# Kernel tuning notes

Hardware: AMD Instinct MI355X
Metric: run time of the kernel (lower is better)

## Reference

```python
import jax, jax.numpy as jnp
import numpy as np

H = 1024  # hidden_size == embedding_size


def setup_inputs() -> dict:
    key = jax.random.key(0)
    ks = jax.random.split(key, 14)
    B, T, L, V = 2, 1, 8192, 50000
    emb_table = jax.random.normal(ks[0], (V, H), jnp.float32)
    emb_table = emb_table.at[0].set(0.0)  # row 0 zeroed as in the torch module
    return {
        "input_ids": jax.random.randint(ks[1], (B, T), 0, V),
        "last_context": jax.random.normal(ks[2], (B, T, H), jnp.float32),
        "last_hidden": jax.random.normal(ks[3], (1, B, H), jnp.float32),
        "encoder_outputs": jax.random.normal(ks[4], (B, L, H), jnp.float32),
        "emb_table": emb_table,
        "w_ih": jax.random.normal(ks[5], (3 * H, 2 * H), jnp.float32) * 0.02,
        "w_hh": jax.random.normal(ks[6], (3 * H, H), jnp.float32) * 0.02,
        "b_ih": jax.random.normal(ks[7], (3 * H,), jnp.float32) * 0.02,
        "b_hh": jax.random.normal(ks[8], (3 * H,), jnp.float32) * 0.02,
        "attn_w": jax.random.normal(ks[9], (H, 2 * H), jnp.float32) * 0.02,
        "attn_b": jax.random.normal(ks[10], (H,), jnp.float32) * 0.02,
        "v": jax.random.normal(ks[11], (H,), jnp.float32),
        "out_w": jax.random.normal(ks[12], (50000, 2 * H), jnp.float32) * 0.02,
        "out_b": jax.random.normal(ks[13], (50000,), jnp.float32) * 0.02,
    }


def _forward(input_ids, last_context, last_hidden, encoder_outputs, emb_table,
             w_ih, w_hh, b_ih, b_hh, attn_w, attn_b, v, out_w, out_b):
    # Embedding lookup (dropout p=0 -> identity)
    embedded = emb_table[input_ids]                      # [B,1,H]
    rnn_in = jnp.concatenate([embedded, last_context], -1)  # [B,1,2H]

    # Single-step, single-layer GRU (torch gate order: r, z, n)
    x = rnn_in[:, 0]                                     # [B,2H]
    h = last_hidden[0]                                   # [B,H]
    gx = x @ w_ih.T + b_ih                               # [B,3H]
    gh = h @ w_hh.T + b_hh                               # [B,3H]
    r = jax.nn.sigmoid(gx[:, :H] + gh[:, :H])
    z = jax.nn.sigmoid(gx[:, H:2 * H] + gh[:, H:2 * H])
    n = jnp.tanh(gx[:, 2 * H:] + r * gh[:, 2 * H:])
    h_new = (1.0 - z) * n + z * h                        # [B,H]
    rnn_output = h_new[:, None, :]                       # [B,1,H]
    hidden = h_new[None]                                 # [1,B,H]

    # Bahdanau 'concat' attention, vectorized over the seq_len loop:
    # energy[b,i] = v . (attn_w @ concat(h_new[b], enc[b,i]) + attn_b)
    w_h, w_e = attn_w[:, :H], attn_w[:, H:]
    e_h = h_new @ w_h.T + attn_b                         # [B,H]
    e_e = jnp.einsum('blh,kh->blk', encoder_outputs, w_e)  # [B,L,H]
    energies = jnp.einsum('blk,k->bl', e_e + e_h[:, None, :], v)  # [B,L]
    attn_weights = jax.nn.softmax(energies, axis=1)      # [B,L]
    context = jnp.einsum('bl,blh->bh', attn_weights, encoder_outputs)[:, None, :]  # [B,1,H]

    # Output projection over concat(rnn_output, context)
    cat = jnp.concatenate([rnn_output, context], -1)     # [B,1,2H]
    output = cat @ out_w.T + out_b                       # [B,1,V]
    return output, context, hidden, embedded, rnn_output


def reference(input_ids, last_context, last_hidden, encoder_outputs, emb_table,
              w_ih, w_hh, b_ih, b_hh, attn_w, attn_b, v, out_w, out_b):
    return _forward(input_ids, last_context, last_hidden, encoder_outputs, emb_table,
                    w_ih, w_hh, b_ih, b_hh, attn_w, attn_b, v, out_w, out_b)
```

## Files before the change

### kernel.cpp

```cpp
#include <hip/hip_runtime.h>

#define H 1024
#define LEN 8192
#define V 50000
#define NTILE 12500
#define NBO 500
#define CHUNK 8
#define NCH (LEN / CHUNK)

__device__ __forceinline__ float dot4(float4 a, float4 b) {
    return a.x * b.x + a.y * b.y + a.z * b.z + a.w * b.w;
}

__device__ __forceinline__ void gld_lds16(const float* g, float* l) {
    __builtin_amdgcn_global_load_lds(
        (const __attribute__((address_space(1))) void*)g,
        (__attribute__((address_space(3))) void*)l, 16, 0, 0);
}

__global__ void k_pre(const float* __restrict__ attn_w,
                      const float* __restrict__ v,
                      float* __restrict__ u,
                      const int* __restrict__ ids,
                      const float* __restrict__ emb,
                      float* __restrict__ out_emb,
                      const float* __restrict__ lctx,
                      const float* __restrict__ lhid,
                      const float* __restrict__ w_ih,
                      const float* __restrict__ w_hh,
                      const float* __restrict__ b_ih,
                      const float* __restrict__ b_hh,
                      float* __restrict__ o_hidden,
                      float* __restrict__ o_rnn) {
    __shared__ float red[16][16];
    __shared__ float lds[3][4][4];
    int bid = blockIdx.x;
    int t   = threadIdx.x;

    if (bid < 64) {
        int kg = t >> 4;
        int hi = t & 15;
        int h  = bid * 16 + hi;
        float acc = 0.f;
#pragma unroll 8
        for (int i = 0; i < 64; ++i) {
            int k = kg * 64 + i;
            acc += v[k] * attn_w[(long)k * (2 * H) + H + h];
        }
        red[kg][hi] = acc;
        __syncthreads();
        if (t < 16) {
            float s = 0.f;
#pragma unroll
            for (int g = 0; g < 16; ++g) s += red[g][t];
            u[bid * 16 + t] = s;
        }
        return;
    }
    if (bid < 72) {
        int idx = (bid - 64) * 256 + t;
        int b = idx >> 10, h = idx & 1023;
        out_emb[idx] = emb[(long)ids[b] * H + h];
        return;
    }

    int hh = bid - 72;
    int kb = t * 8;

    float4 x0a, x0b, x1a, x1b;
    if (kb < H) {
        const float* p0 = emb + (long)ids[0] * H + kb;
        const float* p1 = emb + (long)ids[1] * H + kb;
        x0a = *(const float4*)p0;  x0b = *(const float4*)(p0 + 4);
        x1a = *(const float4*)p1;  x1b = *(const float4*)(p1 + 4);
    } else {
        const float* p0 = lctx + (kb - H);
        const float* p1 = lctx + H + (kb - H);
        x0a = *(const float4*)p0;  x0b = *(const float4*)(p0 + 4);
        x1a = *(const float4*)p1;  x1b = *(const float4*)(p1 + 4);
    }
    int kb2 = t * 4;
    float4 h0 = *(const float4*)(lhid + kb2);
    float4 h1 = *(const float4*)(lhid + H + kb2);

    for (int g = 0; g < 3; ++g) {
        const float* wi = w_ih + ((long)g * H + hh) * (2 * H) + kb;
        const float* wh = w_hh + ((long)g * H + hh) * H + kb2;
        float4 wa = *(const float4*)wi;
        float4 wb = *(const float4*)(wi + 4);
        float4 wc = *(const float4*)wh;
        float a0 = dot4(wa, x0a) + dot4(wb, x0b);
        float a1 = dot4(wa, x1a) + dot4(wb, x1b);
        float c0 = dot4(wc, h0);
        float c1 = dot4(wc, h1);
        for (int off = 32; off; off >>= 1) {
            a0 += __shfl_down(a0, off, 64);
            a1 += __shfl_down(a1, off, 64);
            c0 += __shfl_down(c0, off, 64);
            c1 += __shfl_down(c1, off, 64);
        }
        if ((t & 63) == 0) {
            int w = t >> 6;
            lds[g][w][0] = a0; lds[g][w][1] = a1;
            lds[g][w][2] = c0; lds[g][w][3] = c1;
        }
    }
    __syncthreads();
    if (t == 0) {
        float gx[3][2], gh[3][2];
        for (int g = 0; g < 3; ++g) {
            float s0 = 0, s1 = 0, s2 = 0, s3 = 0;
            for (int w = 0; w < 4; ++w) {
                s0 += lds[g][w][0]; s1 += lds[g][w][1];
                s2 += lds[g][w][2]; s3 += lds[g][w][3];
            }
            float bi = b_ih[g * H + hh], bh = b_hh[g * H + hh];
            gx[g][0] = s0 + bi; gx[g][1] = s1 + bi;
            gh[g][0] = s2 + bh; gh[g][1] = s3 + bh;
        }
        for (int b = 0; b < 2; ++b) {
            float r  = 1.f / (1.f + expf(-(gx[0][b] + gh[0][b])));
            float z  = 1.f / (1.f + expf(-(gx[1][b] + gh[1][b])));
            float n  = tanhf(gx[2][b] + r * gh[2][b]);
            float hp = lhid[b * H + hh];
            float hn = (1.f - z) * n + z * hp;
            o_hidden[b * H + hh] = hn;
            o_rnn[b * H + hh]    = hn;
        }
    }
}

__global__ void __launch_bounds__(256)
k_ctx(const float* __restrict__ enc,
      const float* __restrict__ u,
      float* __restrict__ pvec,
      float* __restrict__ marr,
      float* __restrict__ sarr) {
    __shared__ float erow[CHUNK * H];
    __shared__ float elds[CHUNK];
    int t    = threadIdx.x;
    int lane = t & 63;
    int wv   = t >> 6;
    int b    = blockIdx.x >> 10;
    int ch   = blockIdx.x & 1023;

    const float* src = enc + ((long)b * LEN + (long)ch * CHUNK) * H;
#pragma unroll
    for (int i = 0; i < CHUNK; ++i)
        gld_lds16(src + i * H + t * 4, erow + i * H + t * 4);

    float4 uf[4];
#pragma unroll
    for (int c = 0; c < 4; ++c)
        uf[c] = *(const float4*)(u + c * 256 + lane * 4);

    __syncthreads();

#pragma unroll
    for (int rr = 0; rr < 2; ++rr) {
        int r = wv * 2 + rr;
        float acc = 0.f;
#pragma unroll
        for (int c = 0; c < 4; ++c) {
            float4 ev = *(const float4*)(erow + r * H + c * 256 + lane * 4);
            acc += dot4(ev, uf[c]);
        }
        for (int off = 32; off; off >>= 1) acc += __shfl_down(acc, off, 64);
        if (lane == 0) elds[r] = acc;
    }
    __syncthreads();

    float m = elds[0];
#pragma unroll
    for (int r = 1; r < CHUNK; ++r) m = fmaxf(m, elds[r]);
    float p[CHUNK];
    float s = 0.f;
#pragma unroll
    for (int r = 0; r < CHUNK; ++r) { p[r] = expf(elds[r] - m); s += p[r]; }

    float4 acc = {0.f, 0.f, 0.f, 0.f};
#pragma unroll
    for (int r = 0; r < CHUNK; ++r) {
        float4 ev = *(const float4*)(erow + r * H + t * 4);
        acc.x += p[r] * ev.x; acc.y += p[r] * ev.y;
        acc.z += p[r] * ev.z; acc.w += p[r] * ev.w;
    }
    *(float4*)(pvec + (long)blockIdx.x * H + t * 4) = acc;
    if (t == 0) { marr[blockIdx.x] = m; sarr[blockIdx.x] = s; }
}

__global__ void __launch_bounds__(256)
k_red(const float* __restrict__ pvec,
      const float* __restrict__ marr,
      const float* __restrict__ sarr,
      float* __restrict__ out_ctx) {
    __shared__ float scale[NCH];
    __shared__ float rbuf[4];
    __shared__ float4 part[32][8];
    int t  = threadIdx.x;
    int b  = blockIdx.x >> 5;
    int h0 = (blockIdx.x & 31) * 32;
    const float* mb = marr + b * NCH;
    const float* sb = sarr + b * NCH;

    float m = -3.4e38f;
    for (int i = t; i < NCH; i += 256) m = fmaxf(m, mb[i]);
    for (int off = 32; off; off >>= 1) m = fmaxf(m, __shfl_xor(m, off, 64));
    if ((t & 63) == 0) rbuf[t >> 6] = m;
    __syncthreads();
    m = fmaxf(fmaxf(rbuf[0], rbuf[1]), fmaxf(rbuf[2], rbuf[3]));
    __syncthreads();

    float d = 0.f;
    for (int i = t; i < NCH; i += 256) {
        float sc = expf(mb[i] - m);
        scale[i] = sc;
        d += sc * sb[i];
    }
    for (int off = 32; off; off >>= 1) d += __shfl_xor(d, off, 64);
    if ((t & 63) == 0) rbuf[t >> 6] = d;
    __syncthreads();
    float inv = 1.f / (rbuf[0] + rbuf[1] + rbuf[2] + rbuf[3]);

    int hq    = t & 7;
    int clane = t >> 3;
    const float* pv = pvec + (long)b * NCH * H + h0 + hq * 4;
    float4 acc = {0.f, 0.f, 0.f, 0.f};
#pragma unroll
    for (int k = 0; k < 32; ++k) {
        int c = clane + 32 * k;
        float sc = scale[c];
        float4 p = *(const float4*)(pv + (long)c * H);
        acc.x += sc * p.x; acc.y += sc * p.y;
        acc.z += sc * p.z; acc.w += sc * p.w;
    }
    part[clane][hq] = acc;
    __syncthreads();
    if (t < 8) {
        float4 s4 = {0.f, 0.f, 0.f, 0.f};
#pragma unroll
        for (int c = 0; c < 32; ++c) {
            float4 p = part[c][t];
            s4.x += p.x; s4.y += p.y; s4.z += p.z; s4.w += p.w;
        }
        s4.x *= inv; s4.y *= inv; s4.z *= inv; s4.w *= inv;
        *(float4*)(out_ctx + b * H + h0 + t * 4) = s4;
    }
}

__global__ void __launch_bounds__(256)
k_out(const float* __restrict__ ow,
      const float* __restrict__ ob,
      const float* __restrict__ hnew,
      const float* __restrict__ ctx,
      float* __restrict__ out) {
    __shared__ float cat[2][2 * H];
    __shared__ float wt[2][4 * 2 * H];
    int t    = threadIdx.x;
    int lane = t & 63;
    int wv   = t >> 6;

    {
        float4* c0 = (float4*)cat[0];
        float4* c1 = (float4*)cat[1];
#pragma unroll
        for (int r = 0; r < 2; ++r) {
            int idx = t + r * 256;
            int k   = idx * 4;
            if (k < H) {
                c0[idx] = *(const float4*)(hnew + k);
                c1[idx] = *(const float4*)(hnew + H + k);
            } else {
                c0[idx] = *(const float4*)(ctx + (k - H));
                c1[idx] = *(const float4*)(ctx + H + (k - H));
            }
        }
    }
    {
        const float* src = ow + (long)blockIdx.x * (4 * 2 * H);
#pragma unroll
        for (int i = 0; i < 8; ++i)
            gld_lds16(src + i * 1024 + t * 4, wt[0] + i * 1024 + t * 4);
    }
    __syncthreads();

    const float4* c0 = (const float4*)cat[0];
    const float4* c1 = (const float4*)cat[1];
    int buf = 0;
    for (int T = blockIdx.x; T < NTILE; T += NBO) {
        int Tn = T + NBO;
        if (Tn < NTILE) {
            const float* src = ow + (long)Tn * (4 * 2 * H);
            float* dst = wt[buf ^ 1];
#pragma unroll
            for (int i = 0; i < 8; ++i)
                gld_lds16(src + i * 1024 + t * 4, dst + i * 1024 + t * 4);
        }
        const float4* wr = (const float4*)(wt[buf] + wv * (2 * H));
        float a0 = 0.f, a1 = 0.f;
#pragma unroll
        for (int j = 0; j < 8; ++j) {
            float4 w = wr[lane + 64 * j];
            a0 += dot4(w, c0[lane + 64 * j]);
            a1 += dot4(w, c1[lane + 64 * j]);
        }
        for (int off = 32; off; off >>= 1) {
            a0 += __shfl_down(a0, off, 64);
            a1 += __shfl_down(a1, off, 64);
        }
        if (lane == 0) {
            long row = (long)T * 4 + wv;
            float bb = ob[row];
            out[row]     = a0 + bb;
            out[V + row] = a1 + bb;
        }
        __syncthreads();
        buf ^= 1;
    }
}

extern "C" void kernel_launch(void* const* d_in, const int* in_sizes, int n_in,
                              void* d_out, int out_size, void* d_ws, size_t ws_size,
                              hipStream_t stream) {
    const int*   ids    = (const int*)  d_in[0];
    const float* lctx   = (const float*)d_in[1];
    const float* lhid   = (const float*)d_in[2];
    const float* enc    = (const float*)d_in[3];
    const float* emb    = (const float*)d_in[4];
    const float* w_ih   = (const float*)d_in[5];
    const float* w_hh   = (const float*)d_in[6];
    const float* b_ih   = (const float*)d_in[7];
    const float* b_hh   = (const float*)d_in[8];
    const float* attn_w = (const float*)d_in[9];
    const float* v      = (const float*)d_in[11];
    const float* out_w  = (const float*)d_in[12];
    const float* out_b  = (const float*)d_in[13];

    float* out_f       = (float*)d_out;
    float* o_output    = out_f;
    float* o_context   = out_f + 100000;
    float* o_hidden    = out_f + 102048;
    float* o_embedded  = out_f + 104096;
    float* o_rnn       = out_f + 106144;

    float* ws   = (float*)d_ws;
    float* U    = ws;
    float* MARR = ws + 1024;
    float* SARR = ws + 3072;
    float* PVEC = ws + 5120;

    k_pre<<<1096, 256, 0, stream>>>(attn_w, v, U, ids, emb, o_embedded,
                                    lctx, lhid, w_ih, w_hh, b_ih, b_hh,
                                    o_hidden, o_rnn);
    k_ctx<<<2048, 256, 0, stream>>>(enc, U, PVEC, MARR, SARR);
    k_red<<<64,   256, 0, stream>>>(PVEC, MARR, SARR, o_context);
    k_out<<<NBO,  256, 0, stream>>>(out_w, out_b, o_hidden, o_context,
                                    o_output);
}
```

Before: 108.5 us.

## Split attention-vector kernel and fuse GRU/embedding work into context kernel

Moves the GRU-gate and embedding-copy blocks out of the pre-kernel and into the encoder context kernel, interleaving one GRU block with every two context chunks. Only the small u = v·W_e projection stays in its own tiny launch ahead of it. The GRU's weight streaming now overlaps the encoder streaming within one grid instead of running as a separate serialized kernel. The trade-off is that the GRU blocks share the fused kernel's large LDS footprint, which can limit occupancy, and block-index arithmetic is added.

```diff
diff --git a/kernel.cpp b/kernel.cpp
--- a/kernel.cpp
+++ b/kernel.cpp
@@ -18,131 +18,140 @@
         (__attribute__((address_space(3))) void*)l, 16, 0, 0);
 }
 
-__global__ void k_pre(const float* __restrict__ attn_w,
-                      const float* __restrict__ v,
-                      float* __restrict__ u,
-                      const int* __restrict__ ids,
-                      const float* __restrict__ emb,
-                      float* __restrict__ out_emb,
-                      const float* __restrict__ lctx,
-                      const float* __restrict__ lhid,
-                      const float* __restrict__ w_ih,
-                      const float* __restrict__ w_hh,
-                      const float* __restrict__ b_ih,
-                      const float* __restrict__ b_hh,
-                      float* __restrict__ o_hidden,
-                      float* __restrict__ o_rnn) {
+__global__ void k_u(const float* __restrict__ attn_w,
+                    const float* __restrict__ v,
+                    float* __restrict__ u) {
     __shared__ float red[16][16];
-    __shared__ float lds[3][4][4];
     int bid = blockIdx.x;
     int t   = threadIdx.x;
-
-    if (bid < 64) {
-        int kg = t >> 4;
-        int hi = t & 15;
-        int h  = bid * 16 + hi;
-        float acc = 0.f;
+    int kg  = t >> 4;
+    int hi  = t & 15;
+    int h   = bid * 16 + hi;
+    float acc = 0.f;
 #pragma unroll 8
-        for (int i = 0; i < 64; ++i) {
-            int k = kg * 64 + i;
-            acc += v[k] * attn_w[(long)k * (2 * H) + H + h];
-        }
-        red[kg][hi] = acc;
-        __syncthreads();
-        if (t < 16) {
-            float s = 0.f;
-#pragma unroll
-            for (int g = 0; g < 16; ++g) s += red[g][t];
-            u[bid * 16 + t] = s;
-        }
-        return;
-    }
-    if (bid < 72) {
-        int idx = (bid - 64) * 256 + t;
-        int b = idx >> 10, h = idx & 1023;
-        out_emb[idx] = emb[(long)ids[b] * H + h];
-        return;
-    }
-
-    int hh = bid - 72;
-    int kb = t * 8;
-
-    float4 x0a, x0b, x1a, x1b;
-    if (kb < H) {
-        const float* p0 = emb + (long)ids[0] * H + kb;
-        const float* p1 = emb + (long)ids[1] * H + kb;
-        x0a = *(const float4*)p0;  x0b = *(const float4*)(p0 + 4);
-        x1a = *(const float4*)p1;  x1b = *(const float4*)(p1 + 4);
-    } else {
-        const float* p0 = lctx + (kb - H);
-        const float* p1 = lctx + H + (kb - H);
-        x0a = *(const float4*)p0;  x0b = *(const float4*)(p0 + 4);
-        x1a = *(const float4*)p1;  x1b = *(const float4*)(p1 + 4);
-    }
-    int kb2 = t * 4;
-    float4 h0 = *(const float4*)(lhid + kb2);
-    float4 h1 = *(const float4*)(lhid + H + kb2);
-
-    for (int g = 0; g < 3; ++g) {
-        const float* wi = w_ih + ((long)g * H + hh) * (2 * H) + kb;
-        const float* wh = w_hh + ((long)g * H + hh) * H + kb2;
-        float4 wa = *(const float4*)wi;
-        float4 wb = *(const float4*)(wi + 4);
-        float4 wc = *(const float4*)wh;
-        float a0 = dot4(wa, x0a) + dot4(wb, x0b);
-        float a1 = dot4(wa, x1a) + dot4(wb, x1b);
-        float c0 = dot4(wc, h0);
-        float c1 = dot4(wc, h1);
-        for (int off = 32; off; off >>= 1) {
-            a0 += __shfl_down(a0, off, 64);
-            a1 += __shfl_down(a1, off, 64);
-            c0 += __shfl_down(c0, off, 64);
-            c1 += __shfl_down(c1, off, 64);
-        }
-        if ((t & 63) == 0) {
-            int w = t >> 6;
-            lds[g][w][0] = a0; lds[g][w][1] = a1;
-            lds[g][w][2] = c0; lds[g][w][3] = c1;
-        }
-    }
-    __syncthreads();
-    if (t == 0) {
-        float gx[3][2], gh[3][2];
-        for (int g = 0; g < 3; ++g) {
-            float s0 = 0, s1 = 0, s2 = 0, s3 = 0;
-            for (int w = 0; w < 4; ++w) {
-                s0 += lds[g][w][0]; s1 += lds[g][w][1];
-                s2 += lds[g][w][2]; s3 += lds[g][w][3];
-            }
-            float bi = b_ih[g * H + hh], bh = b_hh[g * H + hh];
-            gx[g][0] = s0 + bi; gx[g][1] = s1 + bi;
-            gh[g][0] = s2 + bh; gh[g][1] = s3 + bh;
-        }
-        for (int b = 0; b < 2; ++b) {
-            float r  = 1.f / (1.f + expf(-(gx[0][b] + gh[0][b])));
-            float z  = 1.f / (1.f + expf(-(gx[1][b] + gh[1][b])));
-            float n  = tanhf(gx[2][b] + r * gh[2][b]);
-            float hp = lhid[b * H + hh];
-            float hn = (1.f - z) * n + z * hp;
-            o_hidden[b * H + hh] = hn;
-            o_rnn[b * H + hh]    = hn;
-        }
+    for (int i = 0; i < 64; ++i) {
+        int k = kg * 64 + i;
+        acc += v[k] * attn_w[(long)k * (2 * H) + H + h];
+    }
+    red[kg][hi] = acc;
+    __syncthreads();
+    if (t < 16) {
+        float s = 0.f;
+#pragma unroll
+        for (int g = 0; g < 16; ++g) s += red[g][t];
+        u[bid * 16 + t] = s;
     }
 }
 
 __global__ void __launch_bounds__(256)
-k_ctx(const float* __restrict__ enc,
-      const float* __restrict__ u,
-      float* __restrict__ pvec,
-      float* __restrict__ marr,
-      float* __restrict__ sarr) {
-    __shared__ float erow[CHUNK * H];
-    __shared__ float elds[CHUNK];
+k_fuse(const float* __restrict__ enc,
+       const float* __restrict__ u,
+       float* __restrict__ pvec,
+       float* __restrict__ marr,
+       float* __restrict__ sarr,
+       const int* __restrict__ ids,
+       const float* __restrict__ emb,
+       const float* __restrict__ lctx,
+       const float* __restrict__ lhid,
+       const float* __restrict__ w_ih,
+       const float* __restrict__ w_hh,
+       const float* __restrict__ b_ih,
+       const float* __restrict__ b_hh,
+       float* __restrict__ o_hidden,
+       float* __restrict__ o_rnn,
+       float* __restrict__ o_embedded) {
+    __shared__ float smem[CHUNK * H + 8];
     int t    = threadIdx.x;
     int lane = t & 63;
     int wv   = t >> 6;
-    int b    = blockIdx.x >> 10;
-    int ch   = blockIdx.x & 1023;
+    int bid  = blockIdx.x;
+
+    if (bid >= 3072) {
+        int idx = (bid - 3072) * 256 + t;
+        int b = idx >> 10, h = idx & 1023;
+        o_embedded[idx] = emb[(long)ids[b] * H + h];
+        return;
+    }
+
+    int r3 = bid % 3;
+    int q3 = bid / 3;
+
+    if (r3 == 2) {
+        int hh = q3;
+        float* glds = smem;
+        int kb = t * 8;
+        float4 x0a, x0b, x1a, x1b;
+        if (kb < H) {
+            const float* p0 = emb + (long)ids[0] * H + kb;
+            const float* p1 = emb + (long)ids[1] * H + kb;
+            x0a = *(const float4*)p0;  x0b = *(const float4*)(p0 + 4);
+            x1a = *(const float4*)p1;  x1b = *(const float4*)(p1 + 4);
+        } else {
+            const float* p0 = lctx + (kb - H);
+            const float* p1 = lctx + H + (kb - H);
+            x0a = *(const float4*)p0;  x0b = *(const float4*)(p0 + 4);
+            x1a = *(const float4*)p1;  x1b = *(const float4*)(p1 + 4);
+        }
+        int kb2 = t * 4;
+        float4 h0 = *(const float4*)(lhid + kb2);
+        float4 h1 = *(const float4*)(lhid + H + kb2);
+
+        for (int g = 0; g < 3; ++g) {
+            const float* wi = w_ih + ((long)g * H + hh) * (2 * H) + kb;
+            const float* wh = w_hh + ((long)g * H + hh) * H + kb2;
+            float4 wa = *(const float4*)wi;
+            float4 wb = *(const float4*)(wi + 4);
+            float4 wc = *(const float4*)wh;
+            float a0 = dot4(wa, x0a) + dot4(wb, x0b);
+            float a1 = dot4(wa, x1a) + dot4(wb, x1b);
+            float c0 = dot4(wc, h0);
+            float c1 = dot4(wc, h1);
+            for (int off = 32; off; off >>= 1) {
+                a0 += __shfl_down(a0, off, 64);
+                a1 += __shfl_down(a1, off, 64);
+                c0 += __shfl_down(c0, off, 64);
+                c1 += __shfl_down(c1, off, 64);
+            }
+            if (lane == 0) {
+                glds[(g * 4 + wv) * 4 + 0] = a0;
+                glds[(g * 4 + wv) * 4 + 1] = a1;
+                glds[(g * 4 + wv) * 4 + 2] = c0;
+                glds[(g * 4 + wv) * 4 + 3] = c1;
+            }
+        }
+        __syncthreads();
+        if (t == 0) {
+            float gx[3][2], gh[3][2];
+            for (int g = 0; g < 3; ++g) {
+                float s0 = 0, s1 = 0, s2 = 0, s3 = 0;
+                for (int w = 0; w < 4; ++w) {
+                    s0 += glds[(g * 4 + w) * 4 + 0];
+                    s1 += glds[(g * 4 + w) * 4 + 1];
+                    s2 += glds[(g * 4 + w) * 4 + 2];
+                    s3 += glds[(g * 4 + w) * 4 + 3];
+                }
+                float bi = b_ih[g * H + hh], bh = b_hh[g * H + hh];
+                gx[g][0] = s0 + bi; gx[g][1] = s1 + bi;
+                gh[g][0] = s2 + bh; gh[g][1] = s3 + bh;
+            }
+            for (int b = 0; b < 2; ++b) {
+                float r  = 1.f / (1.f + expf(-(gx[0][b] + gh[0][b])));
+                float z  = 1.f / (1.f + expf(-(gx[1][b] + gh[1][b])));
+                float n  = tanhf(gx[2][b] + r * gh[2][b]);
+                float hp = lhid[b * H + hh];
+                float hn = (1.f - z) * n + z * hp;
+                o_hidden[b * H + hh] = hn;
+                o_rnn[b * H + hh]    = hn;
+            }
+        }
+        return;
+    }
+
+    int cidx = q3 * 2 + r3;
+    int b    = cidx >> 10;
+    int ch   = cidx & 1023;
+    float* erow = smem;
+    float* elds = smem + CHUNK * H;
 
     const float* src = enc + ((long)b * LEN + (long)ch * CHUNK) * H;
 #pragma unroll
@@ -185,8 +194,8 @@
         acc.x += p[r] * ev.x; acc.y += p[r] * ev.y;
         acc.z += p[r] * ev.z; acc.w += p[r] * ev.w;
     }
-    *(float4*)(pvec + (long)blockIdx.x * H + t * 4) = acc;
-    if (t == 0) { marr[blockIdx.x] = m; sarr[blockIdx.x] = s; }
+    *(float4*)(pvec + (long)cidx * H + t * 4) = acc;
+    if (t == 0) { marr[cidx] = m; sarr[cidx] = s; }
 }
 
 __global__ void __launch_bounds__(256)
@@ -349,11 +358,11 @@
     float* SARR = ws + 3072;
     float* PVEC = ws + 5120;
 
-    k_pre<<<1096, 256, 0, stream>>>(attn_w, v, U, ids, emb, o_embedded,
-                                    lctx, lhid, w_ih, w_hh, b_ih, b_hh,
-                                    o_hidden, o_rnn);
-    k_ctx<<<2048, 256, 0, stream>>>(enc, U, PVEC, MARR, SARR);
-    k_red<<<64,   256, 0, stream>>>(PVEC, MARR, SARR, o_context);
-    k_out<<<NBO,  256, 0, stream>>>(out_w, out_b, o_hidden, o_context,
-                                    o_output);
-}
+    k_u   <<<64,   256, 0, stream>>>(attn_w, v, U);
+    k_fuse<<<3080, 256, 0, stream>>>(enc, U, PVEC, MARR, SARR,
+                                     ids, emb, lctx, lhid, w_ih, w_hh,
+                                     b_ih, b_hh, o_hidden, o_rnn, o_embedded);
+    k_red <<<64,   256, 0, stream>>>(PVEC, MARR, SARR, o_context);
+    k_out <<<NBO,  256, 0, stream>>>(out_w, out_b, o_hidden, o_context,
+                                     o_output);
+}
```

Result: slower. 111.4 us (+2.7%).
